# Optimization experiments

Hardware: AMD Instinct MI355X
Metric: run time of the kernel (lower is better)

Reference implementation:

```python
import jax, jax.numpy as jnp
import numpy as np

WS = 16          # window_size
N = WS * WS      # tokens per window
H = 8            # num_heads
HD = 64          # head_dim
DIM = 512
EPEG_K = 15
PAD = EPEG_K // 2


def _relative_position_index(ws):
    coords = np.stack(np.meshgrid(np.arange(ws), np.arange(ws), indexing='ij'))  # (2, ws, ws)
    flat = coords.reshape(2, -1)                                                 # (2, N)
    rel = flat[:, :, None] - flat[:, None, :]                                    # (2, N, N)
    rel = rel.transpose(1, 2, 0).astype(np.int64)                                # (N, N, 2)
    rel[..., 0] += ws - 1
    rel[..., 1] += ws - 1
    rel[..., 0] *= 2 * ws - 1
    return rel.sum(-1)                                                           # (N, N)

REL_IDX = jnp.asarray(_relative_position_index(WS), dtype=jnp.int32)


def setup_inputs() -> dict:
    key = jax.random.key(0)
    ks = jax.random.split(key, 8)
    B_ = 128
    x = jax.random.normal(ks[0], (B_, N, DIM), dtype=jnp.float32)
    qkv_w = jax.random.normal(ks[1], (3 * H * HD, DIM), dtype=jnp.float32) * 0.02
    qkv_b = jnp.zeros((3 * H * HD,), dtype=jnp.float32)
    pe_w = jax.random.normal(ks[2], (H, 1, EPEG_K, 1), dtype=jnp.float32) * 0.02  # depthwise (15,1) conv
    pe_b = jnp.zeros((H,), dtype=jnp.float32)
    rpb_table = jax.random.normal(ks[3], ((2 * WS - 1) * (2 * WS - 1), H), dtype=jnp.float32) * 0.02
    proj_w = jax.random.normal(ks[4], (DIM, H * HD), dtype=jnp.float32) * 0.02
    proj_b = jnp.zeros((DIM,), dtype=jnp.float32)
    return {"x": x, "qkv_w": qkv_w, "qkv_b": qkv_b, "pe_w": pe_w, "pe_b": pe_b,
            "rpb_table": rpb_table, "proj_w": proj_w, "proj_b": proj_b}


def reference(x, qkv_w, qkv_b, pe_w, pe_b, rpb_table, proj_w, proj_b):
    B_, n, _ = x.shape
    scale = HD ** -0.5
    qkv = (x @ qkv_w.T + qkv_b).reshape(B_, n, 3, H, HD).transpose(2, 0, 3, 1, 4)  # (3,B_,H,N,hd)
    q, k, v = qkv[0] * scale, qkv[1], qkv[2]
    attn = jnp.einsum('bhnd,bhmd->bhnm', q, k)                                    # (B_,H,N,N)
    # epeg: depthwise conv (k,1) over the score map, per head
    pe = jax.lax.conv_general_dilated(
        attn, pe_w, window_strides=(1, 1), padding=((PAD, PAD), (0, 0)),
        dimension_numbers=('NCHW', 'OIHW', 'NCHW'), feature_group_count=H)
    attn = attn + pe + pe_b[None, :, None, None]
    bias = rpb_table[REL_IDX.reshape(-1)].reshape(n, n, H).transpose(2, 0, 1)     # (H,N,N)
    attn = jax.nn.softmax(attn + bias[None], axis=-1)
    out = jnp.einsum('bhnm,bhmd->bnhd', attn, v).reshape(B_, n, H * HD)
    return out @ proj_w.T + proj_b
```

## Files before the change

### kernel.cpp

```cpp
#include <hip/hip_runtime.h>


typedef unsigned short u16;
typedef unsigned int u32;
typedef __attribute__((ext_vector_type(8))) short short8;
typedef __attribute__((ext_vector_type(4))) float f32x4;

__device__ __forceinline__ u16 f2bf(float f) {
  union { float f; u32 u; } v; v.f = f;
  return (u16)((v.u + 0x7FFFu + ((v.u >> 16) & 1u)) >> 16);
}
__device__ __forceinline__ float bf2f(u16 s) {
  union { u32 u; float f; } v; v.u = ((u32)s) << 16;
  return v.f;
}

__device__ __forceinline__ void gl2lds16(const u16* g, u16* l) {
  __builtin_amdgcn_global_load_lds((const __attribute__((address_space(1))) void*)g,
                                   (__attribute__((address_space(3))) void*)l, 16, 0, 0);
}

__device__ __forceinline__ int fragaddr(int frag, int lane) {
  return (frag * 64 + (lane ^ (frag & 7))) * 8;
}

__global__ __launch_bounds__(256) void cvt_all(
    const float* __restrict__ x, const float* __restrict__ w1f,
    const float* __restrict__ w2f, u16* __restrict__ xo,
    u16* __restrict__ w1o, u16* __restrict__ w2o) {
  const int NX = 4194304, NW1 = 196608, NW2 = 65536;
  int i = blockIdx.x * 256 + threadIdx.x;
  const float* src; u16* dst; int j;
  if (i < NX)                  { src = x;   dst = xo;  j = i; }
  else if (i < NX + NW1)       { src = w1f; dst = w1o; j = i - NX; }
  else if (i < NX + NW1 + NW2) { src = w2f; dst = w2o; j = i - NX - NW1; }
  else return;
  float4 f = ((const float4*)src)[j];
  uint2 o;
  o.x = (u32)f2bf(f.x) | ((u32)f2bf(f.y) << 16);
  o.y = (u32)f2bf(f.z) | ((u32)f2bf(f.w) << 16);
  ((uint2*)dst)[j] = o;
}

template <int KDIM>
__device__ __forceinline__ void gemm_core(const u16* __restrict__ A,
                                          const u16* __restrict__ B,
                                          int m0, int n0,
                                          u16* As, u16* Bs, f32x4 acc[4][4]) {
  int tid = threadIdx.x, wave = tid >> 6, lane = tid & 63;
  int wm = wave >> 1, wn = wave & 1;
  int lr = lane >> 3, lc = (lane & 7) * 8;
  const u16* Ag = A + (size_t)(m0 + wave * 32 + lr) * KDIM + lc;
  const u16* Bg = B + (size_t)(n0 + wave * 32 + lr) * KDIM + lc;
  u16* AsW = As + wave * 32 * 64;
  u16* BsW = Bs + wave * 32 * 64;
  for (int k0 = 0; k0 < KDIM; k0 += 64) {
#pragma unroll
    for (int it = 0; it < 4; ++it) {
      gl2lds16(Ag + k0 + it * 8 * KDIM, AsW + it * 8 * 64);
      gl2lds16(Bg + k0 + it * 8 * KDIM, BsW + it * 8 * 64);
    }
    __syncthreads();
    int q8 = (lane >> 4) * 8;
#pragma unroll
    for (int ks = 0; ks < 64; ks += 32) {
      short8 af[4], bf8[4];
#pragma unroll
      for (int t = 0; t < 4; ++t) {
        af[t]  = *(const short8*)(As + (wm * 64 + t * 16 + (lane & 15)) * 64 + ks + q8);
        bf8[t] = *(const short8*)(Bs + (wn * 64 + t * 16 + (lane & 15)) * 64 + ks + q8);
      }
#pragma unroll
      for (int tm = 0; tm < 4; ++tm)
#pragma unroll
        for (int tn = 0; tn < 4; ++tn)
          acc[tm][tn] = __builtin_amdgcn_mfma_f32_16x16x32_bf16(
              af[tm], bf8[tn], acc[tm][tn], 0, 0, 0);
    }
    __syncthreads();
  }
}

__global__ __launch_bounds__(256) void gemm_qkv(
    const u16* __restrict__ A, const u16* __restrict__ B,
    const float* __restrict__ qkvb, u16* __restrict__ qb,
    u16* __restrict__ kb, u16* __restrict__ vb) {
  __shared__ __align__(16) u16 As[128 * 64];
  __shared__ __align__(16) u16 Bs[128 * 64];
  f32x4 acc[4][4];
#pragma unroll
  for (int a = 0; a < 4; ++a)
#pragma unroll
    for (int c = 0; c < 4; ++c) acc[a][c] = (f32x4){0.f, 0.f, 0.f, 0.f};
  int m0 = blockIdx.x * 128, n0 = blockIdx.y * 128;
  gemm_core<512>(A, B, m0, n0, As, Bs, acc);
  int tid = threadIdx.x, wave = tid >> 6, lane = tid & 63;
  int wm = wave >> 1, wn = wave & 1;
#pragma unroll
  for (int tm = 0; tm < 4; ++tm) {
    int rbase = m0 + wm * 64 + tm * 16 + (lane >> 4) * 4;
#pragma unroll
    for (int tn = 0; tn < 4; ++tn) {
      int c = n0 + wn * 64 + tn * 16 + (lane & 15);
      float bv = qkvb[c];
      int which = c >> 9, cc = c & 511;
      int h = cc >> 6, d = cc & 63;
#pragma unroll
      for (int i = 0; i < 4; ++i) {
        int r = rbase + i;
        int b = r >> 8, n = r & 255;
        float v = acc[tm][tn][i] + bv;
        size_t idx = ((size_t)(b * 8 + h) * 256 + n) * 64 + d;
        if (which == 0)      qb[idx] = f2bf(v * 0.125f);
        else if (which == 1) kb[idx] = f2bf(v);
        else                 vb[idx] = f2bf(v);
      }
    }
  }
}

__global__ __launch_bounds__(256) void qconv(u16* __restrict__ qb,
                                             const float* __restrict__ pe_w) {
  __shared__ __align__(16) u16 Ql[256 * 72];
  __shared__ float w[15];
  int bh = blockIdx.x, h = bh & 7, tid = threadIdx.x;
  const uint4* src = (const uint4*)(qb + (size_t)bh * 16384);
#pragma unroll
  for (int it = 0; it < 8; ++it) {
    int idx = tid + it * 256;
    int row = idx >> 3, c = (idx & 7) * 8;
    *(uint4*)(Ql + row * 72 + c) = src[idx];
  }
  if (tid < 15) w[tid] = pe_w[h * 15 + tid] + (tid == 7 ? 1.f : 0.f);
  __syncthreads();
  int dg = (tid & 15) * 4, nb4 = tid >> 4;
  uint2* dst = (uint2*)(qb + (size_t)bh * 16384);
#pragma unroll
  for (int i = 0; i < 16; ++i) {
    int n = nb4 + i * 16;
    float a0 = 0.f, a1 = 0.f, a2 = 0.f, a3 = 0.f;
#pragma unroll
    for (int t = 0; t < 15; ++t) {
      int nn = n + t - 7;
      if (nn < 0 || nn > 255) continue;
      uint2 rv = *(const uint2*)(Ql + nn * 72 + dg);
      float wt = w[t];
      a0 += wt * bf2f(rv.x & 0xffff); a1 += wt * bf2f(rv.x >> 16);
      a2 += wt * bf2f(rv.y & 0xffff); a3 += wt * bf2f(rv.y >> 16);
    }
    uint2 pv;
    pv.x = (u32)f2bf(a0) | ((u32)f2bf(a1) << 16);
    pv.y = (u32)f2bf(a2) | ((u32)f2bf(a3) << 16);
    dst[(n * 64 + dg) >> 2] = pv;
  }
}

__global__ __launch_bounds__(512, 2) void attn_win(
    const u16* __restrict__ qb, const u16* __restrict__ kb,
    const u16* __restrict__ vb, const float* __restrict__ pe_b,
    const float* __restrict__ rpb, u16* __restrict__ attnout) {
  __shared__ __align__(16) u16 KfPs[21504];
  __shared__ __align__(16) u16 Vf[16384];
  __shared__ float biasl[961];
  __shared__ float pebs;

  int bh = blockIdx.x, b = bh >> 3, h = bh & 7;
  int tid = threadIdx.x, wave = tid >> 6, lane = tid & 63;
  int cx = lane & 15, g = lane >> 4;

  const uint4* kg = (const uint4*)(kb + (size_t)bh * 16384);
  const uint4* vg = (const uint4*)(vb + (size_t)bh * 16384);

  uint4 kreg[4];
#pragma unroll
  for (int it = 0; it < 4; ++it) kreg[it] = kg[tid + it * 512];

  u16* Vtmp = KfPs;
#pragma unroll
  for (int it = 0; it < 4; ++it) {
    int idx = tid + it * 512;
    uint4 v = vg[idx];
    int row = idx >> 3, c8 = (idx & 7) * 8;
    *(uint2*)(Vtmp + row * 68 + c8)     = make_uint2(v.x, v.y);
    *(uint2*)(Vtmp + row * 68 + c8 + 4) = make_uint2(v.z, v.w);
  }
  for (int i = tid; i < 961; i += 512) biasl[i] = rpb[i * 8 + h];
  if (tid == 0) pebs = pe_b[h];
  __syncthreads();

#pragma unroll
  for (int it = 0; it < 4; ++it) {
    int o = tid + it * 512;
    int frag = o >> 6, lanep = o & 63;
    int d = (frag >> 3) * 16 + (lanep & 15);
    int mb = (frag & 7) * 32 + (lanep >> 4) * 8;
    uint4 pk;
    pk.x = (u32)Vtmp[(mb + 0) * 68 + d] | ((u32)Vtmp[(mb + 1) * 68 + d] << 16);
    pk.y = (u32)Vtmp[(mb + 2) * 68 + d] | ((u32)Vtmp[(mb + 3) * 68 + d] << 16);
    pk.z = (u32)Vtmp[(mb + 4) * 68 + d] | ((u32)Vtmp[(mb + 5) * 68 + d] << 16);
    pk.w = (u32)Vtmp[(mb + 6) * 68 + d] | ((u32)Vtmp[(mb + 7) * 68 + d] << 16);
    *(uint4*)(Vf + (frag * 64 + (lanep ^ (frag & 7))) * 8) = pk;
  }
  __syncthreads();

  u16* Kf = KfPs;
#pragma unroll
  for (int it = 0; it < 4; ++it) {
    int idx = tid + it * 512;
    int n = idx >> 3, k8 = idx & 7;
    int frag = (n >> 4) * 2 + (k8 >> 2);
    int lanep = (n & 15) + 16 * (k8 & 3);
    *(uint4*)(Kf + (frag * 64 + (lanep ^ (frag & 7))) * 8) = kreg[it];
  }
  __syncthreads();

  u16* Psw = KfPs + 16384 + wave * 640;
  const u16* qgb = qb + (size_t)bh * 16384;

  for (int it2 = 0; it2 < 2; ++it2) {
    int qbase = it2 * 128 + wave * 16;
    const u16* qg = qgb + qbase * 64;
    short8 qf0 = *(const short8*)(qg + cx * 64 + g * 8);
    short8 qf1 = *(const short8*)(qg + cx * 64 + 32 + g * 8);

    float m_run[4] = {-1e30f, -1e30f, -1e30f, -1e30f};
    float l_run[4] = {0.f, 0.f, 0.f, 0.f};
    f32x4 oacc[4];
#pragma unroll
    for (int dt = 0; dt < 4; ++dt) oacc[dt] = (f32x4){0.f, 0.f, 0.f, 0.f};

#pragma unroll
    for (int c = 0; c < 2; ++c) {
      f32x4 acc[8];
#pragma unroll
      for (int mt = 0; mt < 8; ++mt) acc[mt] = (f32x4){0.f, 0.f, 0.f, 0.f};
#pragma unroll
      for (int mt = 0; mt < 8; ++mt) {
        int fr = (c * 8 + mt) * 2;
        short8 k0 = *(const short8*)(Kf + fragaddr(fr, lane));
        short8 k1 = *(const short8*)(Kf + fragaddr(fr + 1, lane));
        acc[mt] = __builtin_amdgcn_mfma_f32_16x16x32_bf16(qf0, k0, acc[mt], 0, 0, 0);
        acc[mt] = __builtin_amdgcn_mfma_f32_16x16x32_bf16(qf1, k1, acc[mt], 0, 0, 0);
      }

      float alpha4[4];
#pragma unroll
      for (int i = 0; i < 4; ++i) {
        int qtok = qbase + g * 4 + i;
        int bbase = ((qtok >> 4) - c * 8 + 15) * 31 + (qtok & 15) - cx + 15;
#pragma unroll
        for (int mt = 0; mt < 8; ++mt) acc[mt][i] += pebs + biasl[bbase - 31 * mt];
        float mx = acc[0][i];
#pragma unroll
        for (int mt = 1; mt < 8; ++mt) mx = fmaxf(mx, acc[mt][i]);
        mx = fmaxf(mx, __shfl_xor(mx, 1));
        mx = fmaxf(mx, __shfl_xor(mx, 2));
        mx = fmaxf(mx, __shfl_xor(mx, 4));
        mx = fmaxf(mx, __shfl_xor(mx, 8));
        float mnew = fmaxf(m_run[i], mx);
        float al = __expf(m_run[i] - mnew);
        float s = 0.f;
#pragma unroll
        for (int mt = 0; mt < 8; ++mt) {
          float e = __expf(acc[mt][i] - mnew);
          acc[mt][i] = e; s += e;
        }
        s += __shfl_xor(s, 1);
        s += __shfl_xor(s, 2);
        s += __shfl_xor(s, 4);
        s += __shfl_xor(s, 8);
        l_run[i] = l_run[i] * al + s;
        m_run[i] = mnew;
        alpha4[i] = al;
      }
#pragma unroll
      for (int dt = 0; dt < 4; ++dt)
#pragma unroll
        for (int i = 0; i < 4; ++i) oacc[dt][i] *= alpha4[i];

#pragma unroll
      for (int kk = 0; kk < 4; ++kk) {
#pragma unroll
        for (int t2 = 0; t2 < 2; ++t2)
#pragma unroll
          for (int i = 0; i < 4; ++i)
            Psw[(g * 4 + i) * 40 + t2 * 16 + cx] = f2bf(acc[kk * 2 + t2][i]);
        short8 pa = *(const short8*)(Psw + cx * 40 + g * 8);
#pragma unroll
        for (int dt = 0; dt < 4; ++dt) {
          short8 vf = *(const short8*)(Vf + fragaddr(dt * 8 + c * 4 + kk, lane));
          oacc[dt] = __builtin_amdgcn_mfma_f32_16x16x32_bf16(pa, vf, oacc[dt], 0, 0, 0);
        }
      }
    }

    float inv4[4];
#pragma unroll
    for (int i = 0; i < 4; ++i) inv4[i] = 1.f / l_run[i];
#pragma unroll
    for (int dt = 0; dt < 4; ++dt)
#pragma unroll
      for (int i = 0; i < 4; ++i)
        attnout[((size_t)b * 256 + qbase + g * 4 + i) * 512 + h * 64 + dt * 16 + cx]
            = f2bf(oacc[dt][i] * inv4[i]);
  }
}

__global__ __launch_bounds__(256) void gemm_proj(
    const u16* __restrict__ A, const u16* __restrict__ B,
    const float* __restrict__ pb, float* __restrict__ out) {
  __shared__ __align__(16) u16 As[128 * 64];
  __shared__ __align__(16) u16 Bs[128 * 64];
  f32x4 acc[4][4];
#pragma unroll
  for (int a = 0; a < 4; ++a)
#pragma unroll
    for (int c = 0; c < 4; ++c) acc[a][c] = (f32x4){0.f, 0.f, 0.f, 0.f};
  int m0 = blockIdx.x * 128, n0 = blockIdx.y * 128;
  gemm_core<512>(A, B, m0, n0, As, Bs, acc);
  int tid = threadIdx.x, wave = tid >> 6, lane = tid & 63;
  int wm = wave >> 1, wn = wave & 1;
#pragma unroll
  for (int tm = 0; tm < 4; ++tm) {
    int rbase = m0 + wm * 64 + tm * 16 + (lane >> 4) * 4;
#pragma unroll
    for (int tn = 0; tn < 4; ++tn) {
      int c = n0 + wn * 64 + tn * 16 + (lane & 15);
      float bv = pb[c];
#pragma unroll
      for (int i = 0; i < 4; ++i)
        out[(size_t)(rbase + i) * 512 + c] = acc[tm][tn][i] + bv;
    }
  }
}

extern "C" void kernel_launch(void* const* d_in, const int* in_sizes, int n_in,
                              void* d_out, int out_size, void* d_ws, size_t ws_size,
                              hipStream_t stream) {
  const float* x      = (const float*)d_in[0];
  const float* qkv_w  = (const float*)d_in[1];
  const float* qkv_b  = (const float*)d_in[2];
  const float* pe_w   = (const float*)d_in[3];
  const float* pe_b   = (const float*)d_in[4];
  const float* rpb    = (const float*)d_in[5];
  const float* proj_w = (const float*)d_in[6];
  const float* proj_b = (const float*)d_in[7];
  float* out = (float*)d_out;
  char* ws = (char*)d_ws;

  size_t off = 0;
  u16* xbf = (u16*)(ws + off); off += (size_t)16777216 * 2;
  u16* w1  = (u16*)(ws + off); off += (size_t)786432 * 2;
  u16* w2  = (u16*)(ws + off); off += (size_t)262144 * 2;
  u16* qb  = (u16*)(ws + off); off += (size_t)16777216 * 2;
  u16* kb  = (u16*)(ws + off); off += (size_t)16777216 * 2;
  u16* vb  = (u16*)(ws + off); off += (size_t)16777216 * 2;

  hipLaunchKernelGGL(cvt_all, dim3(17408), dim3(256), 0, stream,
                     x, qkv_w, proj_w, xbf, w1, w2);
  hipLaunchKernelGGL(gemm_qkv, dim3(256, 12), dim3(256), 0, stream,
                     xbf, w1, qkv_b, qb, kb, vb);
  hipLaunchKernelGGL(qconv, dim3(1024), dim3(256), 0, stream, qb, pe_w);
  hipLaunchKernelGGL(attn_win, dim3(1024), dim3(512), 0, stream,
                     qb, kb, vb, pe_b, rpb, xbf);
  hipLaunchKernelGGL(gemm_proj, dim3(256, 4), dim3(256), 0, stream,
                     xbf, w2, proj_b, out);
}
```

Baseline: 358.6 us.

## Replace GEMMs with 256x256-tile double-buffered pipelined MFMA kernels

Both the QKV and output-projection GEMMs move from a 128x128 tile with 4 waves and a load/compute/sync loop to a 256x256 tile with 8 waves. The new core uses swizzled LDS, double-buffered global-to-LDS staging with explicit vmcnt waits, interleaved barriers, setprio around MFMA bursts, and an XCD-aware block remap. The aim is more data reuse per tile and hiding global load latency behind MFMA work. In exchange it uses 128KB of LDS per block and a large accumulator, which can limit occupancy, and the QKV epilogue is still scattered.

```diff
diff --git a/kernel.cpp b/kernel.cpp
--- a/kernel.cpp
+++ b/kernel.cpp
@@ -42,79 +42,174 @@
   ((uint2*)dst)[j] = o;
 }
 
-template <int KDIM>
-__device__ __forceinline__ void gemm_core(const u16* __restrict__ A,
-                                          const u16* __restrict__ B,
-                                          int m0, int n0,
-                                          u16* As, u16* Bs, f32x4 acc[4][4]) {
+__device__ __forceinline__ void gemm256_core(
+    const u16* __restrict__ A, const u16* __restrict__ B,
+    int m0, int n0, u16* lds, f32x4 acc[8][4]) {
+  const int NT = 8;
   int tid = threadIdx.x, wave = tid >> 6, lane = tid & 63;
-  int wm = wave >> 1, wn = wave & 1;
-  int lr = lane >> 3, lc = (lane & 7) * 8;
-  const u16* Ag = A + (size_t)(m0 + wave * 32 + lr) * KDIM + lc;
-  const u16* Bg = B + (size_t)(n0 + wave * 32 + lr) * KDIM + lc;
-  u16* AsW = As + wave * 32 * 64;
-  u16* BsW = Bs + wave * 32 * 64;
-  for (int k0 = 0; k0 < KDIM; k0 += 64) {
-#pragma unroll
-    for (int it = 0; it < 4; ++it) {
-      gl2lds16(Ag + k0 + it * 8 * KDIM, AsW + it * 8 * 64);
-      gl2lds16(Bg + k0 + it * 8 * KDIM, BsW + it * 8 * 64);
-    }
-    __syncthreads();
-    int q8 = (lane >> 4) * 8;
-#pragma unroll
-    for (int ks = 0; ks < 64; ks += 32) {
-      short8 af[4], bf8[4];
-#pragma unroll
-      for (int t = 0; t < 4; ++t) {
-        af[t]  = *(const short8*)(As + (wm * 64 + t * 16 + (lane & 15)) * 64 + ks + q8);
-        bf8[t] = *(const short8*)(Bs + (wn * 64 + t * 16 + (lane & 15)) * 64 + ks + q8);
-      }
-#pragma unroll
-      for (int tm = 0; tm < 4; ++tm)
-#pragma unroll
-        for (int tn = 0; tn < 4; ++tn)
-          acc[tm][tn] = __builtin_amdgcn_mfma_f32_16x16x32_bf16(
-              af[tm], bf8[tn], acc[tm][tn], 0, 0, 0);
-    }
-    __syncthreads();
-  }
-}
-
-__global__ __launch_bounds__(256) void gemm_qkv(
+  int wm = wave >> 2, wn = wave & 3;
+
+  int ch0 = tid, ch1 = tid + 512;
+  int row0 = ch0 >> 2, row1 = ch1 >> 2;
+  int cg0 = (ch0 & 3) ^ (row0 & 3) ^ ((row0 >> 2) & 3);
+  int cg1 = (ch1 & 3) ^ (row1 & 3) ^ ((row1 >> 2) & 3);
+  const u16* Ag0 = A + (size_t)(m0 + row0) * 512 + cg0 * 8;
+  const u16* Ag1 = A + (size_t)(m0 + row1) * 512 + cg1 * 8;
+  const u16* Bg0 = B + (size_t)(n0 + row0) * 512 + cg0 * 8;
+  const u16* Bg1 = B + (size_t)(n0 + row1) * 512 + cg1 * 8;
+  int ldsu0 = wave * 64 * 8;
+  int ldsu1 = (512 + wave * 64) * 8;
+
+  int frag_off = (lane & 15) * 32 +
+                 (((lane >> 4) ^ (lane & 3) ^ ((lane >> 2) & 3)) << 3);
+  int abase = wm * 4096 + frag_off;
+  int bbase = 8192 + wn * 2048 + frag_off;
+
+#define STAGE(h)                                                             \
+  do {                                                                       \
+    if ((h) < NT * 4) {                                                      \
+      int T_ = (h) >> 2, kh_ = ((h) >> 1) & 1, isB_ = (h) & 1;               \
+      int ko_ = T_ * 64 + kh_ * 32;                                          \
+      u16* d_ = lds + (T_ & 1) * 32768 + kh_ * 16384 + isB_ * 8192;          \
+      gl2lds16((isB_ ? Bg0 : Ag0) + ko_, d_ + ldsu0);                        \
+      gl2lds16((isB_ ? Bg1 : Ag1) + ko_, d_ + ldsu1);                        \
+    }                                                                        \
+  } while (0)
+
+#define LDA(dst, mf, kh, p)                                                  \
+  dst = *(const short8*)(lds + (p) * 32768 + (kh) * 16384 + abase + (mf) * 512)
+#define LDB(dst, nf, kh, p)                                                  \
+  dst = *(const short8*)(lds + (p) * 32768 + (kh) * 16384 + bbase + (nf) * 512)
+
+#define MM16(M0)                                                                                   \
+  __builtin_amdgcn_s_setprio(1);                                                                   \
+  acc[(M0)+0][0] = __builtin_amdgcn_mfma_f32_16x16x32_bf16(a0, b0, acc[(M0)+0][0], 0, 0, 0);       \
+  acc[(M0)+0][1] = __builtin_amdgcn_mfma_f32_16x16x32_bf16(a0, b1, acc[(M0)+0][1], 0, 0, 0);       \
+  acc[(M0)+0][2] = __builtin_amdgcn_mfma_f32_16x16x32_bf16(a0, b2, acc[(M0)+0][2], 0, 0, 0);       \
+  acc[(M0)+0][3] = __builtin_amdgcn_mfma_f32_16x16x32_bf16(a0, b3, acc[(M0)+0][3], 0, 0, 0);       \
+  acc[(M0)+1][0] = __builtin_amdgcn_mfma_f32_16x16x32_bf16(a1, b0, acc[(M0)+1][0], 0, 0, 0);       \
+  acc[(M0)+1][1] = __builtin_amdgcn_mfma_f32_16x16x32_bf16(a1, b1, acc[(M0)+1][1], 0, 0, 0);       \
+  acc[(M0)+1][2] = __builtin_amdgcn_mfma_f32_16x16x32_bf16(a1, b2, acc[(M0)+1][2], 0, 0, 0);       \
+  acc[(M0)+1][3] = __builtin_amdgcn_mfma_f32_16x16x32_bf16(a1, b3, acc[(M0)+1][3], 0, 0, 0);       \
+  acc[(M0)+2][0] = __builtin_amdgcn_mfma_f32_16x16x32_bf16(a2, b0, acc[(M0)+2][0], 0, 0, 0);       \
+  acc[(M0)+2][1] = __builtin_amdgcn_mfma_f32_16x16x32_bf16(a2, b1, acc[(M0)+2][1], 0, 0, 0);       \
+  acc[(M0)+2][2] = __builtin_amdgcn_mfma_f32_16x16x32_bf16(a2, b2, acc[(M0)+2][2], 0, 0, 0);       \
+  acc[(M0)+2][3] = __builtin_amdgcn_mfma_f32_16x16x32_bf16(a2, b3, acc[(M0)+2][3], 0, 0, 0);       \
+  acc[(M0)+3][0] = __builtin_amdgcn_mfma_f32_16x16x32_bf16(a3, b0, acc[(M0)+3][0], 0, 0, 0);       \
+  acc[(M0)+3][1] = __builtin_amdgcn_mfma_f32_16x16x32_bf16(a3, b1, acc[(M0)+3][1], 0, 0, 0);       \
+  acc[(M0)+3][2] = __builtin_amdgcn_mfma_f32_16x16x32_bf16(a3, b2, acc[(M0)+3][2], 0, 0, 0);       \
+  acc[(M0)+3][3] = __builtin_amdgcn_mfma_f32_16x16x32_bf16(a3, b3, acc[(M0)+3][3], 0, 0, 0);       \
+  __builtin_amdgcn_s_setprio(0)
+
+  STAGE(0); STAGE(1); STAGE(2); STAGE(3); STAGE(4);
+  asm volatile("s_waitcnt vmcnt(6)" ::: "memory");
+  __builtin_amdgcn_s_barrier();
+
+#pragma unroll 1
+  for (int kt = 0; kt < NT; ++kt) {
+    int p = kt & 1;
+    int hb = kt * 4 + 5;
+    short8 a0, a1, a2, a3, b0, b1, b2, b3;
+    LDA(a0, 0, 0, p); LDA(a1, 1, 0, p); LDA(a2, 2, 0, p); LDA(a3, 3, 0, p);
+    LDB(b0, 0, 0, p); LDB(b1, 1, 0, p); LDB(b2, 2, 0, p); LDB(b3, 3, 0, p);
+    STAGE(hb);
+    __builtin_amdgcn_s_barrier();
+    asm volatile("s_waitcnt lgkmcnt(0)" ::: "memory");
+    MM16(0);
+    __builtin_amdgcn_s_barrier();
+    LDA(a0, 4, 0, p); LDA(a1, 5, 0, p); LDA(a2, 6, 0, p); LDA(a3, 7, 0, p);
+    STAGE(hb + 1);
+    __builtin_amdgcn_s_barrier();
+    asm volatile("s_waitcnt lgkmcnt(0)" ::: "memory");
+    MM16(4);
+    if (kt == NT - 1) asm volatile("s_waitcnt vmcnt(0)" ::: "memory");
+    else              asm volatile("s_waitcnt vmcnt(6)" ::: "memory");
+    __builtin_amdgcn_s_barrier();
+    LDA(a0, 0, 1, p); LDA(a1, 1, 1, p); LDA(a2, 2, 1, p); LDA(a3, 3, 1, p);
+    LDB(b0, 0, 1, p); LDB(b1, 1, 1, p); LDB(b2, 2, 1, p); LDB(b3, 3, 1, p);
+    STAGE(hb + 2);
+    __builtin_amdgcn_s_barrier();
+    asm volatile("s_waitcnt lgkmcnt(0)" ::: "memory");
+    MM16(0);
+    __builtin_amdgcn_s_barrier();
+    LDA(a0, 4, 1, p); LDA(a1, 5, 1, p); LDA(a2, 6, 1, p); LDA(a3, 7, 1, p);
+    STAGE(hb + 3);
+    __builtin_amdgcn_s_barrier();
+    asm volatile("s_waitcnt lgkmcnt(0)" ::: "memory");
+    MM16(4);
+    if (kt == NT - 2)     asm volatile("s_waitcnt vmcnt(4)" ::: "memory");
+    else if (kt < NT - 2) asm volatile("s_waitcnt vmcnt(6)" ::: "memory");
+    __builtin_amdgcn_s_barrier();
+  }
+#undef STAGE
+#undef LDA
+#undef LDB
+#undef MM16
+}
+
+__global__ __launch_bounds__(512, 2) void gemm_qkv256(
     const u16* __restrict__ A, const u16* __restrict__ B,
     const float* __restrict__ qkvb, u16* __restrict__ qb,
     u16* __restrict__ kb, u16* __restrict__ vb) {
-  __shared__ __align__(16) u16 As[128 * 64];
-  __shared__ __align__(16) u16 Bs[128 * 64];
-  f32x4 acc[4][4];
-#pragma unroll
-  for (int a = 0; a < 4; ++a)
+  __shared__ __align__(16) u16 lds[65536];
+  f32x4 acc[8][4];
+#pragma unroll
+  for (int a = 0; a < 8; ++a)
 #pragma unroll
     for (int c = 0; c < 4; ++c) acc[a][c] = (f32x4){0.f, 0.f, 0.f, 0.f};
-  int m0 = blockIdx.x * 128, n0 = blockIdx.y * 128;
-  gemm_core<512>(A, B, m0, n0, As, Bs, acc);
+  int bid = blockIdx.x;
+  int wg = (bid & 7) * 96 + (bid >> 3);
+  int m0 = (wg / 6) * 256, n0 = (wg % 6) * 256;
+  gemm256_core(A, B, m0, n0, lds, acc);
   int tid = threadIdx.x, wave = tid >> 6, lane = tid & 63;
-  int wm = wave >> 1, wn = wave & 1;
-#pragma unroll
-  for (int tm = 0; tm < 4; ++tm) {
-    int rbase = m0 + wm * 64 + tm * 16 + (lane >> 4) * 4;
-#pragma unroll
-    for (int tn = 0; tn < 4; ++tn) {
-      int c = n0 + wn * 64 + tn * 16 + (lane & 15);
-      float bv = qkvb[c];
-      int which = c >> 9, cc = c & 511;
-      int h = cc >> 6, d = cc & 63;
+  int wm = wave >> 2, wn = wave & 3;
+#pragma unroll
+  for (int nf = 0; nf < 4; ++nf) {
+    int c = n0 + wn * 64 + nf * 16 + (lane & 15);
+    float bv = qkvb[c];
+    int which = c >> 9, cc = c & 511, h = cc >> 6, d = cc & 63;
+#pragma unroll
+    for (int mf = 0; mf < 8; ++mf) {
+      int rbase = m0 + wm * 128 + mf * 16 + (lane >> 4) * 4;
 #pragma unroll
       for (int i = 0; i < 4; ++i) {
         int r = rbase + i;
         int b = r >> 8, n = r & 255;
-        float v = acc[tm][tn][i] + bv;
+        float v = acc[mf][nf][i] + bv;
         size_t idx = ((size_t)(b * 8 + h) * 256 + n) * 64 + d;
         if (which == 0)      qb[idx] = f2bf(v * 0.125f);
         else if (which == 1) kb[idx] = f2bf(v);
         else                 vb[idx] = f2bf(v);
       }
+    }
+  }
+}
+
+__global__ __launch_bounds__(512, 2) void gemm_proj256(
+    const u16* __restrict__ A, const u16* __restrict__ B,
+    const float* __restrict__ pb, float* __restrict__ out) {
+  __shared__ __align__(16) u16 lds[65536];
+  f32x4 acc[8][4];
+#pragma unroll
+  for (int a = 0; a < 8; ++a)
+#pragma unroll
+    for (int c = 0; c < 4; ++c) acc[a][c] = (f32x4){0.f, 0.f, 0.f, 0.f};
+  int bid = blockIdx.x;
+  int wg = (bid & 7) * 32 + (bid >> 3);
+  int m0 = (wg >> 1) * 256, n0 = (wg & 1) * 256;
+  gemm256_core(A, B, m0, n0, lds, acc);
+  int tid = threadIdx.x, wave = tid >> 6, lane = tid & 63;
+  int wm = wave >> 2, wn = wave & 3;
+#pragma unroll
+  for (int nf = 0; nf < 4; ++nf) {
+    int c = n0 + wn * 64 + nf * 16 + (lane & 15);
+    float bv = pb[c];
+#pragma unroll
+    for (int mf = 0; mf < 8; ++mf) {
+      int rbase = m0 + wm * 128 + mf * 16 + (lane >> 4) * 4;
+#pragma unroll
+      for (int i = 0; i < 4; ++i)
+        out[(size_t)(rbase + i) * 512 + c] = acc[mf][nf][i] + bv;
     }
   }
 }
@@ -303,34 +398,6 @@
       for (int i = 0; i < 4; ++i)
         attnout[((size_t)b * 256 + qbase + g * 4 + i) * 512 + h * 64 + dt * 16 + cx]
             = f2bf(oacc[dt][i] * inv4[i]);
-  }
-}
-
-__global__ __launch_bounds__(256) void gemm_proj(
-    const u16* __restrict__ A, const u16* __restrict__ B,
-    const float* __restrict__ pb, float* __restrict__ out) {
-  __shared__ __align__(16) u16 As[128 * 64];
-  __shared__ __align__(16) u16 Bs[128 * 64];
-  f32x4 acc[4][4];
-#pragma unroll
-  for (int a = 0; a < 4; ++a)
-#pragma unroll
-    for (int c = 0; c < 4; ++c) acc[a][c] = (f32x4){0.f, 0.f, 0.f, 0.f};
-  int m0 = blockIdx.x * 128, n0 = blockIdx.y * 128;
-  gemm_core<512>(A, B, m0, n0, As, Bs, acc);
-  int tid = threadIdx.x, wave = tid >> 6, lane = tid & 63;
-  int wm = wave >> 1, wn = wave & 1;
-#pragma unroll
-  for (int tm = 0; tm < 4; ++tm) {
-    int rbase = m0 + wm * 64 + tm * 16 + (lane >> 4) * 4;
-#pragma unroll
-    for (int tn = 0; tn < 4; ++tn) {
-      int c = n0 + wn * 64 + tn * 16 + (lane & 15);
-      float bv = pb[c];
-#pragma unroll
-      for (int i = 0; i < 4; ++i)
-        out[(size_t)(rbase + i) * 512 + c] = acc[tm][tn][i] + bv;
-    }
   }
 }
 
@@ -358,11 +425,11 @@
 
   hipLaunchKernelGGL(cvt_all, dim3(17408), dim3(256), 0, stream,
                      x, qkv_w, proj_w, xbf, w1, w2);
-  hipLaunchKernelGGL(gemm_qkv, dim3(256, 12), dim3(256), 0, stream,
+  hipLaunchKernelGGL(gemm_qkv256, dim3(768), dim3(512), 0, stream,
                      xbf, w1, qkv_b, qb, kb, vb);
   hipLaunchKernelGGL(qconv, dim3(1024), dim3(256), 0, stream, qb, pe_w);
   hipLaunchKernelGGL(attn_win, dim3(1024), dim3(512), 0, stream,
                      qb, kb, vb, pe_b, rpb, xbf);
-  hipLaunchKernelGGL(gemm_proj, dim3(256, 4), dim3(256), 0, stream,
+  hipLaunchKernelGGL(gemm_proj256, dim3(256), dim3(512), 0, stream,
                      xbf, w2, proj_b, out);
 }
```

Result: no change. 364.5 us (+1.7%).
